# Performance work log

Hardware: AMD Instinct MI355X
Metric: run time of the kernel (lower is better)

## Reference

```python
import jax, jax.numpy as jnp
import numpy as np

IN_DIM = 1024
HEAD_DIM = 64
NUM_HEADS = 16
SEQ = 4096


def setup_inputs() -> dict:
    key = jax.random.key(0)
    ks = jax.random.split(key, 7)
    s = 1.0 / np.sqrt(IN_DIM)
    return {
        "h": jax.random.normal(ks[0], (SEQ, IN_DIM), dtype=jnp.float32),
        "Wq": jax.random.uniform(ks[1], (IN_DIM, NUM_HEADS * HEAD_DIM), jnp.float32, -s, s),
        "Wk": jax.random.uniform(ks[2], (IN_DIM, NUM_HEADS * HEAD_DIM), jnp.float32, -s, s),
        "Wv": jax.random.uniform(ks[3], (IN_DIM, NUM_HEADS * HEAD_DIM), jnp.float32, -s, s),
        "bq": jax.random.uniform(ks[4], (NUM_HEADS * HEAD_DIM,), jnp.float32, -s, s),
        "bk": jax.random.uniform(ks[5], (NUM_HEADS * HEAD_DIM,), jnp.float32, -s, s),
        "bv": jax.random.uniform(ks[6], (NUM_HEADS * HEAD_DIM,), jnp.float32, -s, s),
    }


def reference(h, Wq, Wk, Wv, bq, bk, bv):
    n = h.shape[0]
    # QKV projections -> [H, S, D]
    q = (h @ Wq + bq).reshape(n, NUM_HEADS, HEAD_DIM).transpose(1, 0, 2)
    k = (h @ Wk + bk).reshape(n, NUM_HEADS, HEAD_DIM).transpose(1, 0, 2)
    v = (h @ Wv + bv).reshape(n, NUM_HEADS, HEAD_DIM).transpose(1, 0, 2)
    scale = 1.0 / np.sqrt(HEAD_DIM).astype(np.float32)
    scores = jnp.einsum('hsd,htd->hst', q, k) * scale  # [H, S, S]
    probs = jax.nn.softmax(scores, axis=-1)
    out = jnp.einsum('hst,htd->hsd', probs, v)  # [H, S, D]
    return out.transpose(1, 0, 2).reshape(n, NUM_HEADS * HEAD_DIM)
```

## Files before the change

### kernel.cpp

```cpp
#include <hip/hip_runtime.h>
#include <hip/hip_bf16.h>

#define IN_DIM    1024
#define HEAD_DIM  64
#define NUM_HEADS 16
#define SEQ       4096

#define QSCALE 0.18033688011112042f

typedef __bf16 bf16;
typedef __attribute__((ext_vector_type(4))) __bf16 bf16x4;
typedef __attribute__((ext_vector_type(8))) __bf16 bf16x8;
typedef __attribute__((ext_vector_type(4))) float floatx4;
typedef __attribute__((ext_vector_type(16))) float floatx16;
typedef __attribute__((ext_vector_type(4))) unsigned uint32x4;

__device__ __forceinline__ void async16(bf16* lds, const bf16* g) {
    __builtin_amdgcn_global_load_lds(
        (const __attribute__((address_space(1))) unsigned int*)g,
        (__attribute__((address_space(3))) unsigned int*)lds, 16, 0, 0);
}

__device__ __forceinline__ unsigned cvtpk_bf16(float lo, float hi) {
    unsigned r;
    asm("v_cvt_pk_bf16_f32 %0, %1, %2" : "=v"(r) : "v"(lo), "v"(hi));
    return r;
}

__device__ __forceinline__ void permswap(unsigned& a, unsigned& b) {
    asm("v_permlane32_swap_b32 %0, %1" : "+v"(a), "+v"(b));
}


__global__ void mha_conv_h(const float* __restrict__ h, bf16* __restrict__ hb) {
    int i = blockIdx.x * blockDim.x + threadIdx.x;
    float4 v = ((const float4*)h)[i];
    bf16x4 r;
    r[0] = (bf16)v.x; r[1] = (bf16)v.y; r[2] = (bf16)v.z; r[3] = (bf16)v.w;
    ((bf16x4*)hb)[i] = r;
}

__global__ void mha_conv_wt(const float* __restrict__ Wq, const float* __restrict__ Wk,
                            const float* __restrict__ Wv, bf16* __restrict__ Wt) {
    __shared__ bf16 tile[64][65];
    const int mat = blockIdx.z;
    const float* W = (mat == 0) ? Wq : (mat == 1) ? Wk : Wv;
    const int k0 = blockIdx.y * 64, n0 = blockIdx.x * 64;
    const int tn = threadIdx.x & 63, tq = threadIdx.x >> 6;
#pragma unroll
    for (int i = 0; i < 16; ++i) {
        int kk = tq + i * 4;
        tile[kk][tn] = (bf16)W[(size_t)(k0 + kk) * 1024 + n0 + tn];
    }
    __syncthreads();
#pragma unroll
    for (int i = 0; i < 16; ++i) {
        int nn = tq + i * 4;
        Wt[((size_t)mat << 20) + (size_t)(n0 + nn) * 1024 + k0 + tn] = tile[tn][nn];
    }
}

__launch_bounds__(256)
__global__ void mha_qkv_gemm(const bf16* __restrict__ hb, const bf16* __restrict__ Wt,
                             const float* __restrict__ bq, const float* __restrict__ bk,
                             const float* __restrict__ bv,
                             bf16* __restrict__ Qb, bf16* __restrict__ Kb,
                             bf16* __restrict__ Vt) {
    __shared__ __align__(16) bf16 As[128 * 32];
    __shared__ __align__(16) bf16 Bs[128 * 32];

    const int lane = threadIdx.x & 63;
    const int wave = threadIdx.x >> 6;
    const int l16  = lane & 15;
    const int quad = lane >> 4;
    const int wm   = wave & 1;
    const int wn   = wave >> 1;

    const int m0  = blockIdx.x * 128;
    const int n0  = blockIdx.y * 128;
    const int mat = n0 >> 10;
    const int nc0 = n0 & 1023;

    const bf16* Wp = Wt + ((size_t)mat << 20);

    floatx4 acc[4][4] = {};
    const int swz = (l16 >> 1) & 3;

    for (int k0 = 0; k0 < IN_DIM; k0 += 32) {
#pragma unroll
        for (int r = 0; r < 2; ++r) {
            int g = wave * 128 + r * 64 + lane;
            int row = g >> 2, c = g & 3;
            int gc = c ^ ((row >> 1) & 3);
            bf16* ldsbase_a = As + (size_t)(wave * 128 + r * 64) * 8;
            bf16* ldsbase_b = Bs + (size_t)(wave * 128 + r * 64) * 8;
            async16(ldsbase_a, hb + (size_t)(m0 + row) * IN_DIM + k0 + gc * 8);
            async16(ldsbase_b, Wp + (size_t)(nc0 + row) * IN_DIM + k0 + gc * 8);
        }
        __syncthreads();

        bf16x8 af[4], bf[4];
#pragma unroll
        for (int mt = 0; mt < 4; ++mt)
            af[mt] = *(const bf16x8*)(As + (size_t)(wm * 64 + mt * 16 + l16) * 32
                                      + ((quad ^ swz) * 8));
#pragma unroll
        for (int nt = 0; nt < 4; ++nt)
            bf[nt] = *(const bf16x8*)(Bs + (size_t)(wn * 64 + nt * 16 + l16) * 32
                                      + ((quad ^ swz) * 8));
#pragma unroll
        for (int mt = 0; mt < 4; ++mt)
#pragma unroll
            for (int nt = 0; nt < 4; ++nt)
                acc[mt][nt] = __builtin_amdgcn_mfma_f32_16x16x32_bf16(af[mt], bf[nt],
                                                                      acc[mt][nt], 0, 0, 0);
        __syncthreads();
    }

    const float* bias = (mat == 0) ? bq : (mat == 1) ? bk : bv;
#pragma unroll
    for (int nt = 0; nt < 4; ++nt) {
        int nc = nc0 + wn * 64 + nt * 16 + l16;
        float bb = bias[nc];
        int head = nc >> 6, d = nc & 63;
#pragma unroll
        for (int mt = 0; mt < 4; ++mt)
#pragma unroll
            for (int r = 0; r < 4; ++r) {
                int srow = m0 + wm * 64 + mt * 16 + quad * 4 + r;
                float v = acc[mt][nt][r] + bb;
                if (mat == 0)
                    Qb[((size_t)head * SEQ + srow) * HEAD_DIM + d] = (bf16)(v * QSCALE);
                else if (mat == 1)
                    Kb[((size_t)head * SEQ + srow) * HEAD_DIM + d] = (bf16)v;
                else
                    Vt[((size_t)head * HEAD_DIM + d) * SEQ + srow] = (bf16)v;
            }
    }
}

__launch_bounds__(256)
__global__ void mha_attn(const bf16* __restrict__ Qb, const bf16* __restrict__ Kb,
                         const bf16* __restrict__ Vt, float* __restrict__ out) {
    __shared__ __align__(16) bf16 Ks[2][64 * 64];
    __shared__ __align__(16) bf16 Vs[2][64 * 64];

    const int lane = threadIdx.x & 63;
    const int wave = threadIdx.x >> 6;
    const int l31  = lane & 31;
    const int hi   = lane >> 5;

    const int hh = blockIdx.y;
    const int q0 = blockIdx.x * 128 + wave * 32;

    const bf16* Qh = Qb + (size_t)hh * SEQ * HEAD_DIM;
    const bf16* Kh = Kb + (size_t)hh * SEQ * HEAD_DIM;
    const bf16* Vh = Vt + (size_t)hh * HEAD_DIM * SEQ;

    const int sg0   = wave * 64 + lane;
    const int srow0 = sg0 >> 3;
    const int sgc   = (sg0 & 7) ^ (srow0 & 7);

    bf16x8 qf[4];
#pragma unroll
    for (int ks = 0; ks < 4; ++ks)
        qf[ks] = *(const bf16x8*)(Qh + (size_t)(q0 + l31) * HEAD_DIM + ks * 16 + hi * 8);

    bf16x8 vone;
#pragma unroll
    for (int i = 0; i < 8; ++i) vone[i] = (bf16)1.0f;

    floatx16 o0 = {}, o1 = {}, ol = {};
    const int swz = l31 & 7;

#pragma unroll
    for (int r = 0; r < 2; ++r) {
        async16(&Ks[0][(r * 256 + wave * 64) * 8],
                Kh + (size_t)(r * 32 + srow0) * HEAD_DIM + sgc * 8);
        async16(&Vs[0][(r * 256 + wave * 64) * 8],
                Vh + (size_t)(r * 32 + srow0) * SEQ + sgc * 8);
    }
    __syncthreads();

    for (int t0 = 0; t0 < SEQ; t0 += 64) {
        const int cur = (t0 >> 6) & 1, nxt = cur ^ 1;
        if (t0 + 64 < SEQ) {
#pragma unroll
            for (int r = 0; r < 2; ++r) {
                async16(&Ks[nxt][(r * 256 + wave * 64) * 8],
                        Kh + (size_t)(t0 + 64 + r * 32 + srow0) * HEAD_DIM + sgc * 8);
                async16(&Vs[nxt][(r * 256 + wave * 64) * 8],
                        Vh + (size_t)(r * 32 + srow0) * SEQ + t0 + 64 + sgc * 8);
            }
        }

        bf16x8 kf[2][4];
#pragma unroll
        for (int tt = 0; tt < 2; ++tt)
#pragma unroll
            for (int ks = 0; ks < 4; ++ks)
                kf[tt][ks] = *(const bf16x8*)(&Ks[cur][(tt * 32 + l31) * 64
                                              + (((ks * 2 + hi) ^ swz) * 8)]);

        floatx16 s0 = {}, s1 = {};
#pragma unroll
        for (int ks = 0; ks < 4; ++ks)
            s0 = __builtin_amdgcn_mfma_f32_32x32x16_bf16(kf[0][ks], qf[ks], s0, 0, 0, 0);
#pragma unroll
        for (int ks = 0; ks < 4; ++ks)
            s1 = __builtin_amdgcn_mfma_f32_32x32x16_bf16(kf[1][ks], qf[ks], s1, 0, 0, 0);

        bf16x8 vf[2][4];
#pragma unroll
        for (int dt = 0; dt < 2; ++dt)
#pragma unroll
            for (int sl = 0; sl < 4; ++sl)
                vf[dt][sl] = *(const bf16x8*)(&Vs[cur][(dt * 32 + l31) * 64
                                              + (((sl * 2 + hi) ^ swz) * 8)]);

        bf16x8 pa[4];
#pragma unroll
        for (int sl = 0; sl < 4; ++sl) {
            const floatx16 sv = (sl < 2) ? s0 : s1;
            const int rb = 8 * (sl & 1);
            float p0 = __builtin_amdgcn_exp2f(sv[rb + 0]);
            float p1 = __builtin_amdgcn_exp2f(sv[rb + 1]);
            float p2 = __builtin_amdgcn_exp2f(sv[rb + 2]);
            float p3 = __builtin_amdgcn_exp2f(sv[rb + 3]);
            float p4 = __builtin_amdgcn_exp2f(sv[rb + 4]);
            float p5 = __builtin_amdgcn_exp2f(sv[rb + 5]);
            float p6 = __builtin_amdgcn_exp2f(sv[rb + 6]);
            float p7 = __builtin_amdgcn_exp2f(sv[rb + 7]);
            unsigned u0 = cvtpk_bf16(p0, p1);
            unsigned u1 = cvtpk_bf16(p2, p3);
            unsigned u2 = cvtpk_bf16(p4, p5);
            unsigned u3 = cvtpk_bf16(p6, p7);
            permswap(u0, u2);
            permswap(u1, u3);
            uint32x4 w;
            w[0] = u0; w[1] = u1; w[2] = u2; w[3] = u3;
            pa[sl] = __builtin_bit_cast(bf16x8, w);
        }

#pragma unroll
        for (int sl = 0; sl < 4; ++sl) {
            o0 = __builtin_amdgcn_mfma_f32_32x32x16_bf16(pa[sl], vf[0][sl], o0, 0, 0, 0);
            o1 = __builtin_amdgcn_mfma_f32_32x32x16_bf16(pa[sl], vf[1][sl], o1, 0, 0, 0);
            ol = __builtin_amdgcn_mfma_f32_32x32x16_bf16(pa[sl], vone, ol, 0, 0, 0);
        }
        __syncthreads();
    }

#pragma unroll
    for (int r = 0; r < 16; ++r) {
        const int q = q0 + (r & 3) + 8 * (r >> 2) + 4 * hi;
        const float inv = 1.0f / ol[r];
        out[(size_t)q * (NUM_HEADS * HEAD_DIM) + hh * 64 + l31]      = o0[r] * inv;
        out[(size_t)q * (NUM_HEADS * HEAD_DIM) + hh * 64 + 32 + l31] = o1[r] * inv;
    }
}

extern "C" void kernel_launch(void* const* d_in, const int* in_sizes, int n_in,
                              void* d_out, int out_size, void* d_ws, size_t ws_size,
                              hipStream_t stream) {
    const float* h  = (const float*)d_in[0];
    const float* Wq = (const float*)d_in[1];
    const float* Wk = (const float*)d_in[2];
    const float* Wv = (const float*)d_in[3];
    const float* bq = (const float*)d_in[4];
    const float* bk = (const float*)d_in[5];
    const float* bv = (const float*)d_in[6];
    float* out = (float*)d_out;

    char* ws = (char*)d_ws;
    const size_t MB = 1024 * 1024;
    bf16* hb = (bf16*)(ws);
    bf16* Wt = (bf16*)(ws + 8 * MB);
    bf16* Qb = (bf16*)(ws + 14 * MB);
    bf16* Kb = (bf16*)(ws + 22 * MB);
    bf16* Vt = (bf16*)(ws + 30 * MB);

    mha_conv_h<<<(SEQ * IN_DIM / 4) / 256, 256, 0, stream>>>(h, hb);
    mha_conv_wt<<<dim3(16, 16, 3), 256, 0, stream>>>(Wq, Wk, Wv, Wt);
    mha_qkv_gemm<<<dim3(SEQ / 128, (3 * IN_DIM) / 128), 256, 0, stream>>>(
        hb, Wt, bq, bk, bv, Qb, Kb, Vt);
    mha_attn<<<dim3(SEQ / 128, NUM_HEADS), 256, 0, stream>>>(Qb, Kb, Vt, out);
}
```

Before: 211.5 us.

## Widen attention blocks to 8 waves with triple-buffered K/V prefetch

Each attention block now has 512 threads (8 waves) covering 256 queries, so every K/V tile loaded into LDS is shared by twice as many waves. K/V staging moves from a double buffer to a triple buffer with prefetch distance two, gated by explicit vmcnt waits and raw s_barrier calls. A 1D grid remaps block IDs so heads are interleaved, which may help L2 locality. The risks are fewer blocks in the grid (256 instead of 512) and fragile hand-written waitcnt/barrier ordering.

```diff
diff --git a/kernel.cpp b/kernel.cpp
--- a/kernel.cpp
+++ b/kernel.cpp
@@ -139,27 +139,29 @@
     }
 }
 
-__launch_bounds__(256)
+__launch_bounds__(512)
 __global__ void mha_attn(const bf16* __restrict__ Qb, const bf16* __restrict__ Kb,
                          const bf16* __restrict__ Vt, float* __restrict__ out) {
-    __shared__ __align__(16) bf16 Ks[2][64 * 64];
-    __shared__ __align__(16) bf16 Vs[2][64 * 64];
+    __shared__ __align__(16) bf16 Ks[3][64 * 64];
+    __shared__ __align__(16) bf16 Vs[3][64 * 64];
 
     const int lane = threadIdx.x & 63;
     const int wave = threadIdx.x >> 6;
     const int l31  = lane & 31;
     const int hi   = lane >> 5;
 
-    const int hh = blockIdx.y;
-    const int q0 = blockIdx.x * 128 + wave * 32;
+    const int bid = blockIdx.x;
+    const int hh  = 2 * (bid & 7) + ((bid >> 3) & 1);
+    const int qx  = bid >> 4;
+    const int q0  = qx * 256 + wave * 32;
 
     const bf16* Qh = Qb + (size_t)hh * SEQ * HEAD_DIM;
     const bf16* Kh = Kb + (size_t)hh * SEQ * HEAD_DIM;
     const bf16* Vh = Vt + (size_t)hh * HEAD_DIM * SEQ;
 
-    const int sg0   = wave * 64 + lane;
-    const int srow0 = sg0 >> 3;
-    const int sgc   = (sg0 & 7) ^ (srow0 & 7);
+    const int sg   = wave * 64 + lane;
+    const int srow = sg >> 3;
+    const int sgc  = (sg & 7) ^ (srow & 7);
 
     bf16x8 qf[4];
 #pragma unroll
@@ -173,26 +175,26 @@
     floatx16 o0 = {}, o1 = {}, ol = {};
     const int swz = l31 & 7;
 
-#pragma unroll
-    for (int r = 0; r < 2; ++r) {
-        async16(&Ks[0][(r * 256 + wave * 64) * 8],
-                Kh + (size_t)(r * 32 + srow0) * HEAD_DIM + sgc * 8);
-        async16(&Vs[0][(r * 256 + wave * 64) * 8],
-                Vh + (size_t)(r * 32 + srow0) * SEQ + sgc * 8);
-    }
-    __syncthreads();
-
-    for (int t0 = 0; t0 < SEQ; t0 += 64) {
-        const int cur = (t0 >> 6) & 1, nxt = cur ^ 1;
-        if (t0 + 64 < SEQ) {
-#pragma unroll
-            for (int r = 0; r < 2; ++r) {
-                async16(&Ks[nxt][(r * 256 + wave * 64) * 8],
-                        Kh + (size_t)(t0 + 64 + r * 32 + srow0) * HEAD_DIM + sgc * 8);
-                async16(&Vs[nxt][(r * 256 + wave * 64) * 8],
-                        Vh + (size_t)(r * 32 + srow0) * SEQ + t0 + 64 + sgc * 8);
-            }
-        }
+    async16(&Ks[0][wave * 512], Kh + (size_t)srow * HEAD_DIM + sgc * 8);
+    async16(&Vs[0][wave * 512], Vh + (size_t)srow * SEQ + 0 + sgc * 8);
+    async16(&Ks[1][wave * 512], Kh + (size_t)(64 + srow) * HEAD_DIM + sgc * 8);
+    async16(&Vs[1][wave * 512], Vh + (size_t)srow * SEQ + 64 + sgc * 8);
+    asm volatile("s_waitcnt vmcnt(0)" ::: "memory");
+    __builtin_amdgcn_s_barrier();
+
+    int cur = 0;
+    for (int t = 0; t < SEQ / 64; ++t) {
+        int pre = cur + 2; if (pre >= 3) pre -= 3;
+        if (t + 2 < SEQ / 64) {
+            const int tg = (t + 2) * 64;
+            async16(&Ks[pre][wave * 512], Kh + (size_t)(tg + srow) * HEAD_DIM + sgc * 8);
+            async16(&Vs[pre][wave * 512], Vh + (size_t)srow * SEQ + tg + sgc * 8);
+        }
+        if (t < SEQ / 64 - 2)      asm volatile("s_waitcnt vmcnt(4)" ::: "memory");
+        else if (t == SEQ / 64 - 2) asm volatile("s_waitcnt vmcnt(2)" ::: "memory");
+        else                        asm volatile("s_waitcnt vmcnt(0)" ::: "memory");
+        __builtin_amdgcn_s_barrier();
+        asm volatile("" ::: "memory");
 
         bf16x8 kf[2][4];
 #pragma unroll
@@ -248,7 +250,10 @@
             o1 = __builtin_amdgcn_mfma_f32_32x32x16_bf16(pa[sl], vf[1][sl], o1, 0, 0, 0);
             ol = __builtin_amdgcn_mfma_f32_32x32x16_bf16(pa[sl], vone, ol, 0, 0, 0);
         }
-        __syncthreads();
+
+        asm volatile("" ::: "memory");
+        __builtin_amdgcn_s_barrier();
+        cur = cur + 1; if (cur == 3) cur = 0;
     }
 
 #pragma unroll
@@ -284,5 +289,5 @@
     mha_conv_wt<<<dim3(16, 16, 3), 256, 0, stream>>>(Wq, Wk, Wv, Wt);
     mha_qkv_gemm<<<dim3(SEQ / 128, (3 * IN_DIM) / 128), 256, 0, stream>>>(
         hb, Wt, bq, bk, bv, Qb, Kb, Vt);
-    mha_attn<<<dim3(SEQ / 128, NUM_HEADS), 256, 0, stream>>>(Qb, Kb, Vt, out);
-}
+    mha_attn<<<dim3((SEQ / 256) * NUM_HEADS), 512, 0, stream>>>(Qb, Kb, Vt, out);
+}
```

New measurement: 206.5 us. 1.02x faster.
